# Optimization experiments

Hardware: AMD Instinct MI355X
Metric: run time of the kernel (lower is better)

The kernel has to match this reference:

```python
import jax, jax.numpy as jnp
import numpy as np

ALPHA = 0.2   # leaky relu negative slope
EPS = 1e-5    # layernorm eps
NEG = -1e12   # mask value from original code


def gat_layer(x, adj, W, a):
    # x: [N, F_in], adj: [N, N] bool, W: [F_in, F_out], a: [2*F_out, 1]
    F_out = W.shape[1]
    Wh = x @ W                                  # [N, F_out]
    # a^T [Wh_i ; Wh_j] decomposes into f1_i + f2_j (same math as the
    # O(N^2 * 2F) concat in the torch code, without materializing it)
    f1 = Wh @ a[:F_out]                         # [N, 1]
    f2 = Wh @ a[F_out:]                         # [N, 1]
    e = jax.nn.leaky_relu(f1 + f2.T, negative_slope=ALPHA)  # [N, N]
    att = jnp.where(adj, e, NEG)
    att = jax.nn.softmax(att, axis=1)           # dropout p=0.0 -> no-op
    return att @ Wh                             # [N, F_out]


def layernorm(x, g, b):
    mu = jnp.mean(x, axis=-1, keepdims=True)
    var = jnp.var(x, axis=-1, keepdims=True)
    return (x - mu) * jax.lax.rsqrt(var + EPS) * g + b


def setup_inputs() -> dict:
    N, F = 8192, 128
    key = jax.random.key(0)
    ks = jax.random.split(key, 12)
    inp = {
        "input_hs": jax.random.normal(ks[0], (2, N, F), jnp.float32),
        "adjs": jax.random.uniform(ks[1], (2, N, N)) < 0.3,   # bool adjacency
        "MPNN_emb": jax.random.normal(ks[2], (N, F), jnp.float32),
        "query": jax.random.normal(ks[3], (1, F), jnp.float32),
        # learned params (xavier-ish scale)
        "W0": jax.random.normal(ks[4], (F, F), jnp.float32) * (1.414 / np.sqrt(F)),
        "a0": jax.random.normal(ks[5], (2 * F, 1), jnp.float32) * 0.1,
        "W1": jax.random.normal(ks[6], (F, F), jnp.float32) * (1.414 / np.sqrt(F)),
        "a1": jax.random.normal(ks[7], (2 * F, 1), jnp.float32) * 0.1,
        "ln_gamma": jnp.ones((F,), jnp.float32),
        "ln_beta": jnp.zeros((F,), jnp.float32),
        "res": jax.random.normal(ks[8], (1, 1), jnp.float32) * 0.5,
    }
    return inp


def reference(input_hs, adjs, MPNN_emb, query, W0, a0, W1, a1, ln_gamma, ln_beta, res):
    h0 = gat_layer(input_hs[0], adjs[0], W0, a0)   # [N, F]
    h1 = gat_layer(input_hs[1], adjs[1], W1, a1)   # [N, F]
    q = layernorm(query, ln_gamma, ln_beta)        # [1, F]
    w1 = q @ h0.T                                  # [1, N]
    w2 = q @ h1.T
    w3 = q @ MPNN_emb.T
    scores = jax.nn.softmax(jnp.concatenate([w1, w2, w3], axis=0), axis=0)  # [3, N]
    # diag_embed(s) @ H is just per-row scaling s[:, None] * H
    mix = (scores[0][:, None] * h0
           + scores[1][:, None] * h1
           + scores[2][:, None] * MPNN_emb)
    return res * mix + input_hs[0]
```

## Files before the change

kernel.cpp:

```cpp
#include <hip/hip_runtime.h>
#include <hip/hip_bf16.h>
#include <cstdint>


#define N 8192
#define F 128
#define JS 8

typedef __attribute__((ext_vector_type(8))) short short8;
typedef __attribute__((ext_vector_type(8))) unsigned short ushort8;
typedef __attribute__((ext_vector_type(4))) float floatx4;

__device__ inline unsigned int f2bf(float x) {
  unsigned int u = __float_as_uint(x);
  u += 0x7FFFu + ((u >> 16) & 1u);
  return u >> 16;
}


__global__ __launch_bounds__(256) void k0_pack(const int* __restrict__ adj,
                                               unsigned int* __restrict__ mask) {
  const size_t gid = (size_t)blockIdx.x * 256 + threadIdx.x;
  const int4* p = (const int4*)adj + gid * 8;
  unsigned int m = 0;
#pragma unroll
  for (int q = 0; q < 8; ++q) {
    int4 v = p[q];
    m |= (v.x != 0) ? (1u << (q * 4 + 0)) : 0u;
    m |= (v.y != 0) ? (1u << (q * 4 + 1)) : 0u;
    m |= (v.z != 0) ? (1u << (q * 4 + 2)) : 0u;
    m |= (v.w != 0) ? (1u << (q * 4 + 3)) : 0u;
  }
  mask[gid] = m;
}

__global__ __launch_bounds__(128) void k1_wh(
    const float* __restrict__ X2, const float* __restrict__ W0,
    const float* __restrict__ W1, const float* __restrict__ a0,
    const float* __restrict__ a1, unsigned short* __restrict__ Whbt,
    float* __restrict__ f1g, float* __restrict__ f2g) {
  const int l  = blockIdx.y;
  const int i0 = blockIdx.x * 16;
  const int c  = threadIdx.x;
  const float* __restrict__ X = X2 + (size_t)l * N * F + (size_t)i0 * F;
  const float* __restrict__ W = l ? W1 : W0;

  __shared__ __align__(16) float sX[16 * F];
  __shared__ float red[2][2][16];
  {
    const float4* src = (const float4*)X;
    float4* dst = (float4*)sX;
#pragma unroll
    for (int qq = 0; qq < 4; ++qq) dst[qq * 128 + c] = src[qq * 128 + c];
  }
  __syncthreads();

  float acc[16];
#pragma unroll
  for (int r = 0; r < 16; ++r) acc[r] = 0.f;

  for (int f4 = 0; f4 < 32; ++f4) {
    float w0 = W[(f4 * 4 + 0) * F + c];
    float w1 = W[(f4 * 4 + 1) * F + c];
    float w2 = W[(f4 * 4 + 2) * F + c];
    float w3 = W[(f4 * 4 + 3) * F + c];
#pragma unroll
    for (int r = 0; r < 16; ++r) {
      float4 xv = *(const float4*)(&sX[r * F + f4 * 4]);
      acc[r] = fmaf(xv.x, w0, acc[r]);
      acc[r] = fmaf(xv.y, w1, acc[r]);
      acc[r] = fmaf(xv.z, w2, acc[r]);
      acc[r] = fmaf(xv.w, w3, acc[r]);
    }
  }

  {
    unsigned short* wdst = Whbt + (size_t)l * F * N + (size_t)c * N + i0;
    ushort8 u0, u1;
#pragma unroll
    for (int r = 0; r < 8; ++r) {
      u0[r] = (unsigned short)f2bf(acc[r]);
      u1[r] = (unsigned short)f2bf(acc[8 + r]);
    }
    *(ushort8*)wdst = u0;
    *(ushort8*)(wdst + 8) = u1;
  }

  const float* __restrict__ a = l ? a1 : a0;
  const float a1c = a[c], a2c = a[F + c];
  const int w = c >> 6, lane = c & 63;
#pragma unroll
  for (int r = 0; r < 16; ++r) {
    float s1 = acc[r] * a1c;
    float s2 = acc[r] * a2c;
#pragma unroll
    for (int off = 32; off; off >>= 1) {
      s1 += __shfl_down(s1, off);
      s2 += __shfl_down(s2, off);
    }
    if (lane == 0) {
      red[w][0][r] = s1;
      red[w][1][r] = s2;
    }
  }
  __syncthreads();
  if (c < 16)
    f1g[l * N + i0 + c] = red[0][0][c] + red[1][0][c];
  else if (c < 32)
    f2g[l * N + i0 + c - 16] = red[0][1][c - 16] + red[1][1][c - 16];
}

__global__ __launch_bounds__(128) void k3_qln(
    const float* __restrict__ query, const float* __restrict__ gamma,
    const float* __restrict__ beta, float* __restrict__ qln) {
  const int t = threadIdx.x;
  float v = query[t];
  float s = v, sq = v * v;
#pragma unroll
  for (int off = 32; off; off >>= 1) {
    s += __shfl_down(s, off);
    sq += __shfl_down(sq, off);
  }
  __shared__ float sb[4];
  if ((t & 63) == 0) {
    sb[t >> 6] = s;
    sb[2 + (t >> 6)] = sq;
  }
  __syncthreads();
  float S = sb[0] + sb[1], SQ = sb[2] + sb[3];
  float mu = S * (1.f / 128.f);
  float var = SQ * (1.f / 128.f) - mu * mu;
  qln[t] = (v - mu) * rsqrtf(var + 1e-5f) * gamma[t] + beta[t];
}

__device__ inline short8 make_pfrag(float f1v, const float4& fa,
                                    const float4& fb, unsigned int bits,
                                    float& Lacc) {
  float p0, p1, p2, p3, p4, p5, p6, p7, sc;
  sc = f1v + fa.x; sc = fmaxf(sc, 0.2f * sc); p0 = (bits & 1u)   ? __expf(sc) : 0.f;
  sc = f1v + fa.y; sc = fmaxf(sc, 0.2f * sc); p1 = (bits & 2u)   ? __expf(sc) : 0.f;
  sc = f1v + fa.z; sc = fmaxf(sc, 0.2f * sc); p2 = (bits & 4u)   ? __expf(sc) : 0.f;
  sc = f1v + fa.w; sc = fmaxf(sc, 0.2f * sc); p3 = (bits & 8u)   ? __expf(sc) : 0.f;
  sc = f1v + fb.x; sc = fmaxf(sc, 0.2f * sc); p4 = (bits & 16u)  ? __expf(sc) : 0.f;
  sc = f1v + fb.y; sc = fmaxf(sc, 0.2f * sc); p5 = (bits & 32u)  ? __expf(sc) : 0.f;
  sc = f1v + fb.z; sc = fmaxf(sc, 0.2f * sc); p6 = (bits & 64u)  ? __expf(sc) : 0.f;
  sc = f1v + fb.w; sc = fmaxf(sc, 0.2f * sc); p7 = (bits & 128u) ? __expf(sc) : 0.f;
  Lacc += ((p0 + p1) + (p2 + p3)) + ((p4 + p5) + (p6 + p7));
  union { unsigned int u[4]; short8 s8; } r;
  r.u[0] = (__float_as_uint(p0) >> 16) | (__float_as_uint(p1) & 0xFFFF0000u);
  r.u[1] = (__float_as_uint(p2) >> 16) | (__float_as_uint(p3) & 0xFFFF0000u);
  r.u[2] = (__float_as_uint(p4) >> 16) | (__float_as_uint(p5) & 0xFFFF0000u);
  r.u[3] = (__float_as_uint(p6) >> 16) | (__float_as_uint(p7) & 0xFFFF0000u);
  return r.s8;
}

__global__ __launch_bounds__(256) void k2_attn(
    const unsigned short* __restrict__ Whbt, const float* __restrict__ f1g,
    const float* __restrict__ f2g, const unsigned int* __restrict__ mask,
    float* __restrict__ hpart, float* __restrict__ Lpart) {
  const int l  = blockIdx.y;
  const int s  = blockIdx.z;
  const int i0 = blockIdx.x * 128;
  const int t  = threadIdx.x;
  const int wave = t >> 6, lane = t & 63;
  const int lpos = lane & 15, halfk = lane >> 4;
  const int shk = halfk * 8;

  __shared__ __align__(16) unsigned short sB[128][136];

  const unsigned short* __restrict__ WhbL = Whbt + (size_t)l * F * N;
  const float* __restrict__ f2L = f2g + l * N;

  const int rowA = i0 + wave * 32 + lpos;
  const float f1a = f1g[l * N + rowA];
  const float f1b = f1g[l * N + rowA + 16];
  const unsigned int* __restrict__ mrowA = mask + ((size_t)l * N + rowA) * (N / 32);
  const unsigned int* __restrict__ mrowB = mrowA + 16 * (N / 32);
  const float* __restrict__ f2base = f2L + shk;

  const unsigned short* __restrict__ wsrc = WhbL + (size_t)(t >> 1) * N + (t & 1) * 8;
  unsigned short* __restrict__ sdst = &sB[t >> 1][(t & 1) * 8];

  floatx4 acc[2][8];
#pragma unroll
  for (int mt = 0; mt < 2; ++mt)
#pragma unroll
    for (int nt = 0; nt < 8; ++nt) acc[mt][nt] = (floatx4){0.f, 0.f, 0.f, 0.f};
  float Lacc0 = 0.f, Lacc1 = 0.f;

  const int jbeg = s * (N / JS);

  for (int st = 0; st < (N / JS) / 128; ++st) {
    const int jb = jbeg + st * 128;
    uint4 mwA = *(const uint4*)(mrowA + (jb >> 5));
    uint4 mwB = *(const uint4*)(mrowB + (jb >> 5));

    __syncthreads();
#pragma unroll
    for (int r = 0; r < 8; ++r)
      *(uint4*)(sdst + r * 16) = *(const uint4*)(wsrc + jb + r * 16);
    __syncthreads();

#pragma unroll
    for (int s4 = 0; s4 < 4; ++s4) {
      const int j0 = jb + s4 * 32;
      const unsigned int bitsA = (((const unsigned int*)&mwA)[s4] >> shk) & 0xFFu;
      const unsigned int bitsB = (((const unsigned int*)&mwB)[s4] >> shk) & 0xFFu;
      float4 fa = *(const float4*)(f2base + j0);
      float4 fb = *(const float4*)(f2base + j0 + 4);

      short8 af0 = make_pfrag(f1a, fa, fb, bitsA, Lacc0);
      short8 af1 = make_pfrag(f1b, fa, fb, bitsB, Lacc1);

      const unsigned short* bp = &sB[lpos][s4 * 32 + shk];
#pragma unroll
      for (int nt = 0; nt < 8; ++nt) {
        short8 bf = *(const short8*)(bp + nt * 16 * 136);
        acc[0][nt] = __builtin_amdgcn_mfma_f32_16x16x32_bf16(af0, bf, acc[0][nt], 0, 0, 0);
        acc[1][nt] = __builtin_amdgcn_mfma_f32_16x16x32_bf16(af1, bf, acc[1][nt], 0, 0, 0);
      }
    }
  }

  const size_t obase = ((size_t)(l * JS + s) * N + i0) * F;
  const size_t lbase = (size_t)(l * JS + s) * N + i0;
#pragma unroll
  for (int mt = 0; mt < 2; ++mt) {
    const int rb = wave * 32 + mt * 16 + halfk * 4;
#pragma unroll
    for (int nt = 0; nt < 8; ++nt) {
#pragma unroll
      for (int reg = 0; reg < 4; ++reg)
        hpart[obase + (size_t)(rb + reg) * F + nt * 16 + lpos] = acc[mt][nt][reg];
    }
  }
  Lacc0 += __shfl_xor(Lacc0, 16);
  Lacc0 += __shfl_xor(Lacc0, 32);
  Lacc1 += __shfl_xor(Lacc1, 16);
  Lacc1 += __shfl_xor(Lacc1, 32);
  if (halfk == 0) {
    Lpart[lbase + wave * 32 + lpos] = Lacc0;
    Lpart[lbase + wave * 32 + 16 + lpos] = Lacc1;
  }
}

__global__ __launch_bounds__(256) void k4_mix(
    const float* __restrict__ hpart, const float* __restrict__ Lpart,
    const float* __restrict__ MPNN, const float* __restrict__ qln,
    const float* __restrict__ x0, const float* __restrict__ res,
    float* __restrict__ out) {
  const int row  = blockIdx.x * 4 + (threadIdx.x >> 6);
  const int lane = threadIdx.x & 63;
  const int c    = lane * 2;

  float h0x = 0.f, h0y = 0.f, h1x = 0.f, h1y = 0.f, L0 = 0.f, L1 = 0.f;
#pragma unroll
  for (int sx = 0; sx < JS; ++sx) {
    float2 v0 = *(const float2*)&hpart[((size_t)(0 * JS + sx) * N + row) * F + c];
    float2 v1 = *(const float2*)&hpart[((size_t)(1 * JS + sx) * N + row) * F + c];
    h0x += v0.x; h0y += v0.y;
    h1x += v1.x; h1y += v1.y;
    L0 += Lpart[(size_t)(0 * JS + sx) * N + row];
    L1 += Lpart[(size_t)(1 * JS + sx) * N + row];
  }
  const float i0v = 1.f / L0, i1v = 1.f / L1;
  h0x *= i0v; h0y *= i0v;
  h1x *= i1v; h1y *= i1v;

  float2 mv = *(const float2*)&MPNN[(size_t)row * F + c];
  float2 qv = *(const float2*)&qln[c];
  float w1 = qv.x * h0x + qv.y * h0y;
  float w2 = qv.x * h1x + qv.y * h1y;
  float w3 = qv.x * mv.x + qv.y * mv.y;
#pragma unroll
  for (int off = 1; off < 64; off <<= 1) {
    w1 += __shfl_xor(w1, off);
    w2 += __shfl_xor(w2, off);
    w3 += __shfl_xor(w3, off);
  }
  float m = fmaxf(w1, fmaxf(w2, w3));
  float e1 = __expf(w1 - m), e2 = __expf(w2 - m), e3 = __expf(w3 - m);
  float inv = res[0] / (e1 + e2 + e3);
  float2 xr = *(const float2*)&x0[(size_t)row * F + c];
  float2 o;
  o.x = (e1 * h0x + e2 * h1x + e3 * mv.x) * inv + xr.x;
  o.y = (e1 * h0y + e2 * h1y + e3 * mv.y) * inv + xr.y;
  *(float2*)&out[(size_t)row * F + c] = o;
}

extern "C" void kernel_launch(void* const* d_in, const int* in_sizes, int n_in,
                              void* d_out, int out_size, void* d_ws,
                              size_t ws_size, hipStream_t stream) {
  const float* x2    = (const float*)d_in[0];
  const int*   adj   = (const int*)d_in[1];
  const float* mpnn  = (const float*)d_in[2];
  const float* query = (const float*)d_in[3];
  const float* W0    = (const float*)d_in[4];
  const float* a0    = (const float*)d_in[5];
  const float* W1    = (const float*)d_in[6];
  const float* a1    = (const float*)d_in[7];
  const float* gamma = (const float*)d_in[8];
  const float* beta  = (const float*)d_in[9];
  const float* res   = (const float*)d_in[10];

  float* ws = (float*)d_ws;
  unsigned short* Whbt = (unsigned short*)ws;
  unsigned int* maskb  = (unsigned int*)(ws + 1048576);
  float* hpart = ws + 5242880;
  float* f1g   = ws + 22020096;
  float* f2g   = ws + 22036480;
  float* Lpart = ws + 22052864;
  float* qln   = ws + 22183936;
  float* out   = (float*)d_out;

  k0_pack<<<2 * N * (N / 32) / 256, 256, 0, stream>>>(adj, maskb);
  k1_wh<<<dim3(N / 16, 2), 128, 0, stream>>>(x2, W0, W1, a0, a1, Whbt, f1g, f2g);
  k3_qln<<<1, 128, 0, stream>>>(query, gamma, beta, qln);
  k2_attn<<<dim3(N / 128, 2, JS), 256, 0, stream>>>(Whbt, f1g, f2g, maskb,
                                                    hpart, Lpart);
  k4_mix<<<N / 4, 256, 0, stream>>>(hpart, Lpart, mpnn, qln, x2, res, out);
}
```

Baseline: 838.4 us.

## Double-buffer Wh tiles in LDS with register prefetch in attention kernel

```diff
diff --git a/kernel.cpp b/kernel.cpp
--- a/kernel.cpp
+++ b/kernel.cpp
@@ -154,7 +154,7 @@
   return r.s8;
 }
 
-__global__ __launch_bounds__(256) void k2_attn(
+__global__ __launch_bounds__(256, 3) void k2_attn(
     const unsigned short* __restrict__ Whbt, const float* __restrict__ f1g,
     const float* __restrict__ f2g, const unsigned int* __restrict__ mask,
     float* __restrict__ hpart, float* __restrict__ Lpart) {
@@ -166,7 +166,7 @@
   const int lpos = lane & 15, halfk = lane >> 4;
   const int shk = halfk * 8;
 
-  __shared__ __align__(16) unsigned short sB[128][136];
+  __shared__ __align__(16) unsigned short sB[2][128][68];
 
   const unsigned short* __restrict__ WhbL = Whbt + (size_t)l * F * N;
   const float* __restrict__ f2L = f2g + l * N;
@@ -178,8 +178,11 @@
   const unsigned int* __restrict__ mrowB = mrowA + 16 * (N / 32);
   const float* __restrict__ f2base = f2L + shk;
 
-  const unsigned short* __restrict__ wsrc = WhbL + (size_t)(t >> 1) * N + (t & 1) * 8;
-  unsigned short* __restrict__ sdst = &sB[t >> 1][(t & 1) * 8];
+  const int ch = t >> 1;
+  const int hh = (t & 1) * 32;
+  const unsigned short* __restrict__ wsrc = WhbL + (size_t)ch * N + hh;
+  unsigned short* __restrict__ sd0 = &sB[0][ch][hh];
+  unsigned short* __restrict__ sd1 = &sB[1][ch][hh];
 
   floatx4 acc[2][8];
 #pragma unroll
@@ -190,36 +193,70 @@
 
   const int jbeg = s * (N / JS);
 
-  for (int st = 0; st < (N / JS) / 128; ++st) {
-    const int jb = jbeg + st * 128;
-    uint4 mwA = *(const uint4*)(mrowA + (jb >> 5));
-    uint4 mwB = *(const uint4*)(mrowB + (jb >> 5));
-
-    __syncthreads();
-#pragma unroll
-    for (int r = 0; r < 8; ++r)
-      *(uint4*)(sdst + r * 16) = *(const uint4*)(wsrc + jb + r * 16);
-    __syncthreads();
-
-#pragma unroll
-    for (int s4 = 0; s4 < 4; ++s4) {
-      const int j0 = jb + s4 * 32;
-      const unsigned int bitsA = (((const unsigned int*)&mwA)[s4] >> shk) & 0xFFu;
-      const unsigned int bitsB = (((const unsigned int*)&mwB)[s4] >> shk) & 0xFFu;
+  {
+    uint4 r0 = *(const uint4*)(wsrc + jbeg);
+    uint4 r1 = *(const uint4*)(wsrc + jbeg + 8);
+    uint4 r2 = *(const uint4*)(wsrc + jbeg + 16);
+    uint4 r3 = *(const uint4*)(wsrc + jbeg + 24);
+    *(uint4*)(sd0 + 0)  = r0;
+    *(uint4*)(sd0 + 8)  = r1;
+    *(uint4*)(sd0 + 16) = r2;
+    *(uint4*)(sd0 + 24) = r3;
+  }
+  uint4 mcA = *(const uint4*)(mrowA + (jbeg >> 5));
+  uint4 mcB = *(const uint4*)(mrowB + (jbeg >> 5));
+  uint4 mnA = mcA, mnB = mcB;
+  __syncthreads();
+
+  for (int st = 0; st < 16; ++st) {
+    const int j0s = jbeg + st * 64;
+    const bool havenext = (st < 15);
+    uint4 n0, n1, n2, n3;
+    if (havenext) {
+      n0 = *(const uint4*)(wsrc + j0s + 64);
+      n1 = *(const uint4*)(wsrc + j0s + 72);
+      n2 = *(const uint4*)(wsrc + j0s + 80);
+      n3 = *(const uint4*)(wsrc + j0s + 88);
+    }
+    if (((st & 1) == 0) && (st + 2 < 16)) {
+      mnA = *(const uint4*)(mrowA + ((j0s + 128) >> 5));
+      mnB = *(const uint4*)(mrowB + ((j0s + 128) >> 5));
+    }
+
+    const unsigned short* __restrict__ bp = &sB[st & 1][0][0] + lpos * 68 + shk;
+#pragma unroll
+    for (int s2 = 0; s2 < 2; ++s2) {
+      const int j0 = j0s + s2 * 32;
+      const unsigned int wArow = (st & 1) ? (s2 ? mcA.w : mcA.z)
+                                          : (s2 ? mcA.y : mcA.x);
+      const unsigned int wBrow = (st & 1) ? (s2 ? mcB.w : mcB.z)
+                                          : (s2 ? mcB.y : mcB.x);
+      const unsigned int bitsA = (wArow >> shk) & 0xFFu;
+      const unsigned int bitsB = (wBrow >> shk) & 0xFFu;
       float4 fa = *(const float4*)(f2base + j0);
       float4 fb = *(const float4*)(f2base + j0 + 4);
 
       short8 af0 = make_pfrag(f1a, fa, fb, bitsA, Lacc0);
       short8 af1 = make_pfrag(f1b, fa, fb, bitsB, Lacc1);
 
-      const unsigned short* bp = &sB[lpos][s4 * 32 + shk];
+      const unsigned short* bq = bp + s2 * 32;
 #pragma unroll
       for (int nt = 0; nt < 8; ++nt) {
-        short8 bf = *(const short8*)(bp + nt * 16 * 136);
+        short8 bf = *(const short8*)(bq + nt * 16 * 68);
         acc[0][nt] = __builtin_amdgcn_mfma_f32_16x16x32_bf16(af0, bf, acc[0][nt], 0, 0, 0);
         acc[1][nt] = __builtin_amdgcn_mfma_f32_16x16x32_bf16(af1, bf, acc[1][nt], 0, 0, 0);
       }
     }
+
+    if (havenext) {
+      unsigned short* nd = (st & 1) ? sd0 : sd1;
+      *(uint4*)(nd + 0)  = n0;
+      *(uint4*)(nd + 8)  = n1;
+      *(uint4*)(nd + 16) = n2;
+      *(uint4*)(nd + 24) = n3;
+    }
+    if ((st & 1) && st < 15) { mcA = mnA; mcB = mnB; }
+    __syncthreads();
   }
 
   const size_t obase = ((size_t)(l * JS + s) * N + i0) * F;
```

Result: slower. 904.6 us (+7.9%).
